# Kernel optimization log

Measured on AMD Instinct MI355X. Metric: run time of the kernel, lower is better.

Reference implementation:

```python
import math
import jax, jax.numpy as jnp
import numpy as np

B, T, C, H = 2, 1024, 1024, 16
D = C // H          # head_dim = 64
ROPE_M = 32         # min(head_dim//2, 64)
FB_M = 32
ROPE_BASE = 10000.0


def setup_inputs() -> dict:
    key = jax.random.key(0)
    ks = jax.random.split(key, 8)
    x = jax.random.normal(ks[0], (B, T, C), dtype=jnp.float32)
    # default coords: per-token position, d_coord=1
    coords = jnp.broadcast_to(jnp.arange(T, dtype=jnp.float32)[None, :, None], (B, T, 1))
    # c_attn / c_proj linear params (torch Linear: y = x @ W.T + b)
    W_attn = jax.random.normal(ks[1], (3 * C, C), dtype=jnp.float32) * (1.0 / math.sqrt(C))
    b_attn = jnp.zeros((3 * C,), dtype=jnp.float32)
    W_proj = jax.random.normal(ks[2], (C, C), dtype=jnp.float32) * (1.0 / math.sqrt(C))
    b_proj = jnp.zeros((C,), dtype=jnp.float32)
    # RoPE freq bank, kind='log': exp(linspace(log(1/base), 0, m)) replicated over d_coord
    steps = jnp.exp(jnp.linspace(math.log(1.0 / ROPE_BASE), 0.0, ROPE_M)).astype(jnp.float32)
    W_rope = steps[:, None]  # [m, d_coord=1]
    # Fourier-bias bank, kind='gaussian', sigma=1.0
    W_fb = jax.random.normal(ks[3], (FB_M, 1), dtype=jnp.float32)
    # betas are zero-init nn.Parameters; use small random values so bias path is exercised
    beta_cos = jax.random.normal(ks[4], (FB_M,), dtype=jnp.float32) * 0.1
    beta_sin = jax.random.normal(ks[5], (FB_M,), dtype=jnp.float32) * 0.1
    return {"x": x, "coords": coords, "W_attn": W_attn, "b_attn": b_attn,
            "W_proj": W_proj, "b_proj": b_proj, "W_rope": W_rope, "W_fb": W_fb,
            "beta_cos": beta_cos, "beta_sin": beta_sin}


def _rope_rotate(z, c, s):
    # z: [B,H,T,D]; c,s: [B,1,T,ROPE_M]; rotates first 2*ROPE_M channels pairwise
    zr = z[..., :2 * ROPE_M].reshape(*z.shape[:-1], ROPE_M, 2)
    y0 = zr[..., 0] * c - zr[..., 1] * s
    y1 = zr[..., 0] * s + zr[..., 1] * c
    y = jnp.stack((y0, y1), axis=-1).reshape(*z.shape[:-1], 2 * ROPE_M)
    return jnp.concatenate([y, z[..., 2 * ROPE_M:]], axis=-1)


def reference(x, coords, W_attn, b_attn, W_proj, b_proj, W_rope, W_fb, beta_cos, beta_sin):
    qkv = x @ W_attn.T + b_attn                      # [B,T,3C]
    q, k, v = jnp.split(qkv, 3, axis=-1)
    to_heads = lambda z: z.reshape(B, T, H, D).transpose(0, 2, 1, 3)  # [B,H,T,D]
    q, k, v = to_heads(q), to_heads(k), to_heads(v)
    # Iron RoPE: theta = coords @ W_rope.T -> [B,T,ROPE_M]
    theta = coords @ W_rope.T
    c = jnp.cos(theta)[:, None]                      # [B,1,T,ROPE_M]
    s = jnp.sin(theta)[:, None]
    q = _rope_rotate(q, c, s)
    k = _rope_rotate(k, c, s)
    att = jnp.einsum('bhqd,bhkd->bhqk', q, k) * (1.0 / math.sqrt(D))
    # relative Fourier bias (shared across heads)
    delta = coords[:, :, None, :] - coords[:, None, :, :]   # [B,Tq,Tk,1]
    S = jnp.einsum('bqkd,md->bqkm', delta, W_fb)            # [B,Tq,Tk,FB_M]
    bias = (jnp.cos(S) * beta_cos + jnp.sin(S) * beta_sin).sum(-1)  # [B,Tq,Tk]
    att = att + (1.0 / math.sqrt(FB_M)) * bias[:, None]     # [B,H,Tq,Tk]
    # non-causal: mask buffer is all ones -> no masking; dropout p=0 -> identity
    att = jax.nn.softmax(att, axis=-1)
    y = jnp.einsum('bhqk,bhkd->bhqd', att, v)
    y = y.transpose(0, 2, 1, 3).reshape(B, T, C)
    y = y @ W_proj.T + b_proj
    return x + y
```

## Files before the change

### kernel.cpp

```cpp
#include <hip/hip_runtime.h>
#include <math.h>

#define Bc 2
#define Tc 1024
#define Cc 1024
#define Hc 16
#define Dc 64
#define DE 128

typedef unsigned short u16;
typedef __attribute__((ext_vector_type(8))) short bf16x8;
typedef __attribute__((ext_vector_type(4))) float f32x4;

#define QSCALE 0.1803368801111243f
#define FIXED_M 24.0f

static __device__ inline u16 f2b(float f) {
    unsigned u = __float_as_uint(f);
    u = (u + 0x7fffu + ((u >> 16) & 1u)) >> 16;
    return (u16)u;
}
static __device__ inline float b2f(u16 h) {
    return __uint_as_float((unsigned)h << 16);
}

typedef __attribute__((address_space(1))) const unsigned int g_u32;
typedef __attribute__((address_space(3))) unsigned int l_u32;
static __device__ __forceinline__ void gll16(const void* g, void* l) {
    __builtin_amdgcn_global_load_lds((g_u32*)g, (l_u32*)l, 16, 0, 0);
}

__global__ __launch_bounds__(256) void cast_all(
    const float* __restrict__ x, const float* __restrict__ wa, const float* __restrict__ wp,
    u16* __restrict__ xb, u16* __restrict__ wab, u16* __restrict__ wpb)
{
    const int NX = Bc * Tc * Cc;
    const int NA = 3 * Cc * Cc;
    int i = (blockIdx.x * 256 + threadIdx.x) * 4;
    const float* src; u16* dst; int off;
    if (i < NX)            { src = x;  dst = xb;  off = i; }
    else if (i < NX + NA)  { src = wa; dst = wab; off = i - NX; }
    else                   { src = wp; dst = wpb; off = i - NX - NA; }
    float4 v = *(const float4*)(src + off);
    ushort4 o;
    o.x = f2b(v.x); o.y = f2b(v.y); o.z = f2b(v.z); o.w = f2b(v.w);
    *(ushort4*)(dst + off) = o;
}

template<int TM, int TN, int WR, int WC, bool OUT_BF16>
__global__ __launch_bounds__(256) void gemm_abt(
    const u16* __restrict__ A, const u16* __restrict__ Bm,
    const float* __restrict__ bias, const float* __restrict__ resid,
    float* __restrict__ outf, u16* __restrict__ outb, int M, int N, int K)
{
    constexpr int WTM = TM / WR;
    constexpr int WTN = TN / WC;
    constexpr int FI = WTM / 16;
    constexpr int FJ = WTN / 16;
    constexpr int ITA = TM / 32;
    constexpr int ITB = TN / 32;
    __shared__ u16 ldsA[2][TM * 64];
    __shared__ u16 ldsB[2][TN * 64];
    const int tid  = threadIdx.x;
    const int wave = tid >> 6;
    const int lane = tid & 63;
    const int l15  = lane & 15;
    const int quad = lane >> 4;
    const int wm = wave / WC;
    const int wn = wave % WC;
    const int tm = blockIdx.y * TM;
    const int tn = blockIdx.x * TN;

    f32x4 acc[FI][FJ] = {};

    auto stage = [&](int buf, int k0) {
#pragma unroll
        for (int it = 0; it < ITA; ++it) {
            int p = it * 256 + tid;
            int row = p >> 3;
            int c = ((p & 7) ^ (row & 7)) * 8;
            gll16(A + (size_t)(tm + row) * K + k0 + c,
                  &ldsA[buf][(it * 256 + (wave << 6)) * 8]);
        }
#pragma unroll
        for (int it = 0; it < ITB; ++it) {
            int p = it * 256 + tid;
            int row = p >> 3;
            int c = ((p & 7) ^ (row & 7)) * 8;
            gll16(Bm + (size_t)(tn + row) * K + k0 + c,
                  &ldsB[buf][(it * 256 + (wave << 6)) * 8]);
        }
    };

    const int NK = K >> 6;
    stage(0, 0);
    for (int ki = 0; ki < NK; ++ki) {
        const int buf = ki & 1;
        __syncthreads();
        if (ki + 1 < NK) stage(buf ^ 1, (ki + 1) << 6);
#pragma unroll
        for (int kk = 0; kk < 2; ++kk) {
            bf16x8 af[FI], bf[FJ];
#pragma unroll
            for (int i = 0; i < FI; ++i) {
                int row = wm * WTM + i * 16 + l15;
                int slot = (kk * 4 + quad) ^ (row & 7);
                af[i] = *(const bf16x8*)&ldsA[buf][row * 64 + slot * 8];
            }
#pragma unroll
            for (int j = 0; j < FJ; ++j) {
                int row = wn * WTN + j * 16 + l15;
                int slot = (kk * 4 + quad) ^ (row & 7);
                bf[j] = *(const bf16x8*)&ldsB[buf][row * 64 + slot * 8];
            }
#pragma unroll
            for (int i = 0; i < FI; ++i)
#pragma unroll
                for (int j = 0; j < FJ; ++j)
                    acc[i][j] = __builtin_amdgcn_mfma_f32_16x16x32_bf16(af[i], bf[j], acc[i][j], 0, 0, 0);
        }
    }

#pragma unroll
    for (int i = 0; i < FI; ++i) {
        int row = tm + wm * WTM + i * 16 + quad * 4;
#pragma unroll
        for (int j = 0; j < FJ; ++j) {
            int col = tn + wn * WTN + j * 16 + l15;
            float bb = bias[col];
#pragma unroll
            for (int r = 0; r < 4; ++r) {
                float v = acc[i][j][r] + bb;
                if (resid) v += resid[(size_t)(row + r) * N + col];
                if (OUT_BF16) outb[(size_t)(row + r) * N + col] = f2b(v);
                else          outf[(size_t)(row + r) * N + col] = v;
            }
        }
    }
}

__global__ __launch_bounds__(256) void prep_kernel(
    const u16* __restrict__ qkv, const float* __restrict__ coords,
    const float* __restrict__ W_rope, const float* __restrict__ W_fb,
    const float* __restrict__ bcos, const float* __restrict__ bsin,
    u16* __restrict__ qe, u16* __restrict__ ke, u16* __restrict__ vt)
{
    const int bt = blockIdx.x;
    const int b = bt >> 10;
    const int t = bt & (Tc - 1);
    const float coord = coords[bt];
    const int tid = threadIdx.x;
    const u16* row = qkv + (size_t)bt * 3072;
    const int e  = tid * 4;
    const int h  = e >> 6;
    const int d0 = e & 63;
    const int m0 = d0 >> 1;

    float th0 = coord * W_rope[m0];
    float th1 = coord * W_rope[m0 + 1];
    float s0 = sinf(th0), c0 = cosf(th0);
    float s1 = sinf(th1), c1 = cosf(th1);

    float q0 = b2f(row[e]), q1 = b2f(row[e + 1]), q2 = b2f(row[e + 2]), q3 = b2f(row[e + 3]);
    float k0 = b2f(row[1024 + e]), k1 = b2f(row[1025 + e]), k2 = b2f(row[1026 + e]), k3 = b2f(row[1027 + e]);
    float v0 = b2f(row[2048 + e]), v1 = b2f(row[2049 + e]), v2 = b2f(row[2050 + e]), v3 = b2f(row[2051 + e]);

    size_t qb = ((size_t)(b * Hc + h) * Tc + t) * DE + d0;
    qe[qb + 0] = f2b((q0 * c0 - q1 * s0) * QSCALE);
    qe[qb + 1] = f2b((q0 * s0 + q1 * c0) * QSCALE);
    qe[qb + 2] = f2b((q2 * c1 - q3 * s1) * QSCALE);
    qe[qb + 3] = f2b((q2 * s1 + q3 * c1) * QSCALE);
    ke[qb + 0] = f2b(k0 * c0 - k1 * s0);
    ke[qb + 1] = f2b(k0 * s0 + k1 * c0);
    ke[qb + 2] = f2b(k2 * c1 - k3 * s1);
    ke[qb + 3] = f2b(k2 * s1 + k3 * c1);

    size_t vb = ((size_t)(b * Hc + h) * Dc + d0) * Tc + t;
    vt[vb]          = f2b(v0);
    vt[vb + Tc]     = f2b(v1);
    vt[vb + 2 * Tc] = f2b(v2);
    vt[vb + 3 * Tc] = f2b(v3);

    {
        const int hh = tid >> 4;
        const int s  = tid & 15;
        const int m  = 2 * s;
        float thf0 = coord * W_fb[m],     thf1 = coord * W_fb[m + 1];
        float sn0 = sinf(thf0), cn0 = cosf(thf0);
        float sn1 = sinf(thf1), cn1 = cosf(thf1);
        float bc0 = bcos[m], bs0 = bsin[m], bc1 = bcos[m + 1], bs1 = bsin[m + 1];
        const float SC = 1.41421356237f * QSCALE;
        unsigned u1 = (unsigned)f2b((bc0 * cn0 + bs0 * sn0) * SC) |
                      ((unsigned)f2b((bc1 * cn1 + bs1 * sn1) * SC) << 16);
        unsigned u2 = (unsigned)f2b((bc0 * sn0 - bs0 * cn0) * SC) |
                      ((unsigned)f2b((bc1 * sn1 - bs1 * cn1) * SC) << 16);
        unsigned cp = (unsigned)f2b(cn0) | ((unsigned)f2b(cn1) << 16);
        unsigned sp = (unsigned)f2b(sn0) | ((unsigned)f2b(sn1) << 16);
        size_t base = ((size_t)(b * Hc + hh) * Tc + t) * DE + 64;
        *(unsigned*)&qe[base + m]      = u1;
        *(unsigned*)&qe[base + 32 + m] = u2;
        *(unsigned*)&ke[base + m]      = cp;
        *(unsigned*)&ke[base + 32 + m] = sp;
    }
}

__global__ __launch_bounds__(256) void attn_kernel(
    const u16* __restrict__ qe, const u16* __restrict__ ke,
    const u16* __restrict__ vt, u16* __restrict__ yb)
{
    __shared__ u16 ldsK[2][64 * 128];
    __shared__ u16 ldsV[2][64 * 64];
    __shared__ u16 plds[4][16][72];
    const int tid  = threadIdx.x;
    const int wave = tid >> 6;
    const int lane = tid & 63;
    const int l15  = lane & 15;
    const int quad = lane >> 4;
    const int qt = blockIdx.x * 64;
    const int h  = blockIdx.y;
    const int b  = blockIdx.z;

    const u16* Q  = qe + ((size_t)(b * Hc + h) * Tc) * DE;
    const u16* Kp = ke + ((size_t)(b * Hc + h) * Tc) * DE;
    const u16* Vp = vt + ((size_t)(b * Hc + h) * Dc) * Tc;

    bf16x8 qf[4];
    {
        const u16* qrow = Q + (size_t)(qt + wave * 16 + l15) * DE + quad * 8;
#pragma unroll
        for (int c = 0; c < 4; ++c) qf[c] = *(const bf16x8*)(qrow + c * 32);
    }

    auto stageKV = [&](int buf, int kt) {
#pragma unroll
        for (int it = 0; it < 4; ++it) {
            int p = it * 256 + tid;
            int row = p >> 4;
            int c = (p & 15) ^ (row & 15);
            gll16(Kp + (size_t)(kt + row) * DE + c * 8,
                  &ldsK[buf][(it * 256 + (wave << 6)) * 8]);
        }
#pragma unroll
        for (int it = 0; it < 2; ++it) {
            int p = it * 256 + tid;
            int row = p >> 3;
            int c = (p & 7) ^ (row & 7);
            gll16(Vp + (size_t)row * Tc + kt + c * 8,
                  &ldsV[buf][(it * 256 + (wave << 6)) * 8]);
        }
    };

    f32x4 o[4] = {};
    float lrow[4] = {0.f, 0.f, 0.f, 0.f};

    stageKV(0, 0);
    for (int ki = 0; ki < Tc / 64; ++ki) {
        const int buf = ki & 1;
        __syncthreads();
        if (ki + 1 < Tc / 64) stageKV(buf ^ 1, (ki + 1) * 64);

        f32x4 sf[4] = {};
#pragma unroll
        for (int f = 0; f < 4; ++f) {
#pragma unroll
            for (int c = 0; c < 4; ++c) {
                int row = f * 16 + l15;
                int slot = (c * 4 + quad) ^ (row & 15);
                bf16x8 kf = *(const bf16x8*)&ldsK[buf][row * 128 + slot * 8];
                sf[f] = __builtin_amdgcn_mfma_f32_16x16x32_bf16(qf[c], kf, sf[f], 0, 0, 0);
            }
        }
        float psum[4] = {0.f, 0.f, 0.f, 0.f};
#pragma unroll
        for (int f = 0; f < 4; ++f)
#pragma unroll
            for (int r = 0; r < 4; ++r) {
                float p = __builtin_amdgcn_exp2f(sf[f][r] - FIXED_M);
                u16 tp = (u16)(__float_as_uint(p) >> 16);
                plds[wave][quad * 4 + r][f * 16 + l15] = tp;
                psum[r] += b2f(tp);
            }
#pragma unroll
        for (int r = 0; r < 4; ++r) {
            float v = psum[r];
#pragma unroll
            for (int off = 1; off < 16; off <<= 1) v += __shfl_xor(v, off);
            lrow[r] += v;
        }

#pragma unroll
        for (int c = 0; c < 2; ++c) {
            bf16x8 pa = *(const bf16x8*)&plds[wave][l15][c * 32 + quad * 8];
#pragma unroll
            for (int df = 0; df < 4; ++df) {
                int row = df * 16 + l15;
                int slot = (c * 4 + quad) ^ (row & 7);
                bf16x8 vf = *(const bf16x8*)&ldsV[buf][row * 64 + slot * 8];
                o[df] = __builtin_amdgcn_mfma_f32_16x16x32_bf16(pa, vf, o[df], 0, 0, 0);
            }
        }
    }

    float rl[4];
#pragma unroll
    for (int r = 0; r < 4; ++r) rl[r] = 1.0f / lrow[r];
#pragma unroll
    for (int df = 0; df < 4; ++df)
#pragma unroll
        for (int r = 0; r < 4; ++r) {
            int t = qt + wave * 16 + quad * 4 + r;
            int d = df * 16 + l15;
            yb[((size_t)b * Tc + t) * Cc + h * Dc + d] = f2b(o[df][r] * rl[r]);
        }
}

extern "C" void kernel_launch(void* const* d_in, const int* in_sizes, int n_in,
                              void* d_out, int out_size, void* d_ws, size_t ws_size,
                              hipStream_t stream) {
    const float* x      = (const float*)d_in[0];
    const float* coords = (const float*)d_in[1];
    const float* W_attn = (const float*)d_in[2];
    const float* b_attn = (const float*)d_in[3];
    const float* W_proj = (const float*)d_in[4];
    const float* b_proj = (const float*)d_in[5];
    const float* W_rope = (const float*)d_in[6];
    const float* W_fb   = (const float*)d_in[7];
    const float* bcos   = (const float*)d_in[8];
    const float* bsin   = (const float*)d_in[9];
    float* out = (float*)d_out;

    char* w = (char*)d_ws;
    const size_t MB = 1024 * 1024;
    u16* xb     = (u16*)(w + 0);
    u16* wab    = (u16*)(w + 4 * MB);
    u16* wpb    = (u16*)(w + 10 * MB);
    u16* qkvb16 = (u16*)(w + 12 * MB);
    u16* qext   = (u16*)(w + 24 * MB);
    u16* kext   = (u16*)(w + 32 * MB);
    u16* vtw    = (u16*)(w + 40 * MB);
    u16* yb     = (u16*)(w + 44 * MB);

    const int NALL = (Bc * Tc * Cc + 3 * Cc * Cc + Cc * Cc) / 4;
    cast_all<<<NALL / 256, 256, 0, stream>>>(x, W_attn, W_proj, xb, wab, wpb);

    dim3 g1(3 * Cc / 128, Bc * Tc / 128);
    gemm_abt<128, 128, 2, 2, true><<<g1, 256, 0, stream>>>(
        xb, wab, b_attn, nullptr, nullptr, qkvb16, Bc * Tc, 3 * Cc, Cc);

    prep_kernel<<<Bc * Tc, 256, 0, stream>>>(qkvb16, coords, W_rope, W_fb, bcos, bsin, qext, kext, vtw);

    dim3 g2(Tc / 64, Hc, Bc);
    attn_kernel<<<g2, 256, 0, stream>>>(qext, kext, vtw, yb);

    dim3 g3(Cc / 64, Bc * Tc / 64);
    gemm_abt<64, 64, 2, 2, false><<<g3, 256, 0, stream>>>(
        yb, wpb, b_proj, x, out, nullptr, Bc * Tc, Cc, Cc);
}
```

Measured before the change: 176.4 us.

## Fuse RoPE and QKV scatter into QKV GEMM epilogue, enlarge proj tile

Moves RoPE rotation, Q scaling and the V transpose into the QKV GEMM epilogue, using a precomputed cos/sin table and a lane shuffle to fetch each pair partner. This removes the intermediate bf16 qkv buffer and the separate prep pass that re-read it. A small prep_tables kernel now builds the rotation table and the Fourier-bias extension columns. The output projection GEMM also moves from 64x64 to 128x64 tiles. The epilogue now issues scattered 2-byte stores into transposed and strided layouts, which may coalesce poorly.

```diff
diff --git a/kernel.cpp b/kernel.cpp
--- a/kernel.cpp
+++ b/kernel.cpp
@@ -47,11 +47,51 @@
     *(ushort4*)(dst + off) = o;
 }
 
-template<int TM, int TN, int WR, int WC, bool OUT_BF16>
+__global__ __launch_bounds__(256) void prep_tables(
+    const float* __restrict__ coords, const float* __restrict__ W_rope,
+    const float* __restrict__ W_fb, const float* __restrict__ bcos,
+    const float* __restrict__ bsin, float2* __restrict__ ctab,
+    u16* __restrict__ qe, u16* __restrict__ ke)
+{
+    const int bt = blockIdx.x;
+    const int b = bt >> 10;
+    const int t = bt & (Tc - 1);
+    const float coord = coords[bt];
+    const int tid = threadIdx.x;
+
+    if (tid < 32) {
+        float th = coord * W_rope[tid];
+        ctab[bt * 32 + tid] = make_float2(cosf(th), sinf(th));
+    }
+
+    const int hh = tid >> 4;
+    const int s  = tid & 15;
+    const int m  = 2 * s;
+    float thf0 = coord * W_fb[m],     thf1 = coord * W_fb[m + 1];
+    float sn0 = sinf(thf0), cn0 = cosf(thf0);
+    float sn1 = sinf(thf1), cn1 = cosf(thf1);
+    float bc0 = bcos[m], bs0 = bsin[m], bc1 = bcos[m + 1], bs1 = bsin[m + 1];
+    const float SC = 1.41421356237f * QSCALE;
+    unsigned u1 = (unsigned)f2b((bc0 * cn0 + bs0 * sn0) * SC) |
+                  ((unsigned)f2b((bc1 * cn1 + bs1 * sn1) * SC) << 16);
+    unsigned u2 = (unsigned)f2b((bc0 * sn0 - bs0 * cn0) * SC) |
+                  ((unsigned)f2b((bc1 * sn1 - bs1 * cn1) * SC) << 16);
+    unsigned cp = (unsigned)f2b(cn0) | ((unsigned)f2b(cn1) << 16);
+    unsigned sp = (unsigned)f2b(sn0) | ((unsigned)f2b(sn1) << 16);
+    size_t base = ((size_t)(b * Hc + hh) * Tc + t) * DE + 64;
+    *(unsigned*)&qe[base + m]      = u1;
+    *(unsigned*)&qe[base + 32 + m] = u2;
+    *(unsigned*)&ke[base + m]      = cp;
+    *(unsigned*)&ke[base + 32 + m] = sp;
+}
+
+template<int TM, int TN, int WR, int WC, int MODE>
 __global__ __launch_bounds__(256) void gemm_abt(
     const u16* __restrict__ A, const u16* __restrict__ Bm,
     const float* __restrict__ bias, const float* __restrict__ resid,
-    float* __restrict__ outf, u16* __restrict__ outb, int M, int N, int K)
+    float* __restrict__ outf, const float2* __restrict__ ctab,
+    u16* __restrict__ qe, u16* __restrict__ ke, u16* __restrict__ vt,
+    int M, int N, int K)
 {
     constexpr int WTM = TM / WR;
     constexpr int WTN = TN / WC;
@@ -121,86 +161,52 @@
         }
     }
 
-#pragma unroll
-    for (int i = 0; i < FI; ++i) {
-        int row = tm + wm * WTM + i * 16 + quad * 4;
-#pragma unroll
-        for (int j = 0; j < FJ; ++j) {
-            int col = tn + wn * WTN + j * 16 + l15;
-            float bb = bias[col];
+    if (MODE == 0) {
+#pragma unroll
+        for (int i = 0; i < FI; ++i) {
+            int row = tm + wm * WTM + i * 16 + quad * 4;
+#pragma unroll
+            for (int j = 0; j < FJ; ++j) {
+                int col = tn + wn * WTN + j * 16 + l15;
+                float bb = bias[col];
+#pragma unroll
+                for (int r = 0; r < 4; ++r) {
+                    float v = acc[i][j][r] + bb;
+                    if (resid) v += resid[(size_t)(row + r) * N + col];
+                    outf[(size_t)(row + r) * N + col] = v;
+                }
+            }
+        }
+    } else {
+        const int sec = tn >> 10;
+#pragma unroll
+        for (int i = 0; i < FI; ++i) {
 #pragma unroll
             for (int r = 0; r < 4; ++r) {
-                float v = acc[i][j][r] + bb;
-                if (resid) v += resid[(size_t)(row + r) * N + col];
-                if (OUT_BF16) outb[(size_t)(row + r) * N + col] = f2b(v);
-                else          outf[(size_t)(row + r) * N + col] = v;
-            }
-        }
-    }
-}
-
-__global__ __launch_bounds__(256) void prep_kernel(
-    const u16* __restrict__ qkv, const float* __restrict__ coords,
-    const float* __restrict__ W_rope, const float* __restrict__ W_fb,
-    const float* __restrict__ bcos, const float* __restrict__ bsin,
-    u16* __restrict__ qe, u16* __restrict__ ke, u16* __restrict__ vt)
-{
-    const int bt = blockIdx.x;
-    const int b = bt >> 10;
-    const int t = bt & (Tc - 1);
-    const float coord = coords[bt];
-    const int tid = threadIdx.x;
-    const u16* row = qkv + (size_t)bt * 3072;
-    const int e  = tid * 4;
-    const int h  = e >> 6;
-    const int d0 = e & 63;
-    const int m0 = d0 >> 1;
-
-    float th0 = coord * W_rope[m0];
-    float th1 = coord * W_rope[m0 + 1];
-    float s0 = sinf(th0), c0 = cosf(th0);
-    float s1 = sinf(th1), c1 = cosf(th1);
-
-    float q0 = b2f(row[e]), q1 = b2f(row[e + 1]), q2 = b2f(row[e + 2]), q3 = b2f(row[e + 3]);
-    float k0 = b2f(row[1024 + e]), k1 = b2f(row[1025 + e]), k2 = b2f(row[1026 + e]), k3 = b2f(row[1027 + e]);
-    float v0 = b2f(row[2048 + e]), v1 = b2f(row[2049 + e]), v2 = b2f(row[2050 + e]), v3 = b2f(row[2051 + e]);
-
-    size_t qb = ((size_t)(b * Hc + h) * Tc + t) * DE + d0;
-    qe[qb + 0] = f2b((q0 * c0 - q1 * s0) * QSCALE);
-    qe[qb + 1] = f2b((q0 * s0 + q1 * c0) * QSCALE);
-    qe[qb + 2] = f2b((q2 * c1 - q3 * s1) * QSCALE);
-    qe[qb + 3] = f2b((q2 * s1 + q3 * c1) * QSCALE);
-    ke[qb + 0] = f2b(k0 * c0 - k1 * s0);
-    ke[qb + 1] = f2b(k0 * s0 + k1 * c0);
-    ke[qb + 2] = f2b(k2 * c1 - k3 * s1);
-    ke[qb + 3] = f2b(k2 * s1 + k3 * c1);
-
-    size_t vb = ((size_t)(b * Hc + h) * Dc + d0) * Tc + t;
-    vt[vb]          = f2b(v0);
-    vt[vb + Tc]     = f2b(v1);
-    vt[vb + 2 * Tc] = f2b(v2);
-    vt[vb + 3 * Tc] = f2b(v3);
-
-    {
-        const int hh = tid >> 4;
-        const int s  = tid & 15;
-        const int m  = 2 * s;
-        float thf0 = coord * W_fb[m],     thf1 = coord * W_fb[m + 1];
-        float sn0 = sinf(thf0), cn0 = cosf(thf0);
-        float sn1 = sinf(thf1), cn1 = cosf(thf1);
-        float bc0 = bcos[m], bs0 = bsin[m], bc1 = bcos[m + 1], bs1 = bsin[m + 1];
-        const float SC = 1.41421356237f * QSCALE;
-        unsigned u1 = (unsigned)f2b((bc0 * cn0 + bs0 * sn0) * SC) |
-                      ((unsigned)f2b((bc1 * cn1 + bs1 * sn1) * SC) << 16);
-        unsigned u2 = (unsigned)f2b((bc0 * sn0 - bs0 * cn0) * SC) |
-                      ((unsigned)f2b((bc1 * sn1 - bs1 * cn1) * SC) << 16);
-        unsigned cp = (unsigned)f2b(cn0) | ((unsigned)f2b(cn1) << 16);
-        unsigned sp = (unsigned)f2b(sn0) | ((unsigned)f2b(sn1) << 16);
-        size_t base = ((size_t)(b * Hc + hh) * Tc + t) * DE + 64;
-        *(unsigned*)&qe[base + m]      = u1;
-        *(unsigned*)&qe[base + 32 + m] = u2;
-        *(unsigned*)&ke[base + m]      = cp;
-        *(unsigned*)&ke[base + 32 + m] = sp;
+                int grow = tm + wm * WTM + i * 16 + quad * 4 + r;
+                int b = grow >> 10, tl = grow & (Tc - 1);
+#pragma unroll
+                for (int j = 0; j < FJ; ++j) {
+                    int col = tn + wn * WTN + j * 16 + l15;
+                    int cw = col & (Cc - 1);
+                    int h = cw >> 6, d = cw & 63;
+                    float v = acc[i][j][r] + bias[col];
+                    if (sec == 2) {
+                        vt[((size_t)(b * Hc + h) * Dc + d) * Tc + tl] = f2b(v);
+                    } else {
+                        float2 cs = ctab[grow * 32 + (d >> 1)];
+                        float p = __shfl_xor(v, 1);
+                        float rot = (d & 1) ? (p * cs.y + v * cs.x)
+                                            : (v * cs.x - p * cs.y);
+                        if (sec == 0) {
+                            qe[((size_t)(b * Hc + h) * Tc + tl) * DE + d] = f2b(rot * QSCALE);
+                        } else {
+                            ke[((size_t)(b * Hc + h) * Tc + tl) * DE + d] = f2b(rot);
+                        }
+                    }
+                }
+            }
+        }
     }
 }
 
@@ -331,28 +337,31 @@
 
     char* w = (char*)d_ws;
     const size_t MB = 1024 * 1024;
-    u16* xb     = (u16*)(w + 0);
-    u16* wab    = (u16*)(w + 4 * MB);
-    u16* wpb    = (u16*)(w + 10 * MB);
-    u16* qkvb16 = (u16*)(w + 12 * MB);
-    u16* qext   = (u16*)(w + 24 * MB);
-    u16* kext   = (u16*)(w + 32 * MB);
-    u16* vtw    = (u16*)(w + 40 * MB);
-    u16* yb     = (u16*)(w + 44 * MB);
+    u16*    xb   = (u16*)(w + 0);
+    u16*    wab  = (u16*)(w + 4 * MB);
+    u16*    wpb  = (u16*)(w + 10 * MB);
+    float2* ctab = (float2*)(w + 12 * MB);
+    u16*    qext = (u16*)(w + 13 * MB);
+    u16*    kext = (u16*)(w + 21 * MB);
+    u16*    vtw  = (u16*)(w + 29 * MB);
+    u16*    yb   = (u16*)(w + 33 * MB);
 
     const int NALL = (Bc * Tc * Cc + 3 * Cc * Cc + Cc * Cc) / 4;
     cast_all<<<NALL / 256, 256, 0, stream>>>(x, W_attn, W_proj, xb, wab, wpb);
 
+    prep_tables<<<Bc * Tc, 256, 0, stream>>>(coords, W_rope, W_fb, bcos, bsin,
+                                             ctab, qext, kext);
+
     dim3 g1(3 * Cc / 128, Bc * Tc / 128);
-    gemm_abt<128, 128, 2, 2, true><<<g1, 256, 0, stream>>>(
-        xb, wab, b_attn, nullptr, nullptr, qkvb16, Bc * Tc, 3 * Cc, Cc);
-
-    prep_kernel<<<Bc * Tc, 256, 0, stream>>>(qkvb16, coords, W_rope, W_fb, bcos, bsin, qext, kext, vtw);
+    gemm_abt<128, 128, 2, 2, 1><<<g1, 256, 0, stream>>>(
+        xb, wab, b_attn, nullptr, nullptr, ctab, qext, kext, vtw,
+        Bc * Tc, 3 * Cc, Cc);
 
     dim3 g2(Tc / 64, Hc, Bc);
     attn_kernel<<<g2, 256, 0, stream>>>(qext, kext, vtw, yb);
 
-    dim3 g3(Cc / 64, Bc * Tc / 64);
-    gemm_abt<64, 64, 2, 2, false><<<g3, 256, 0, stream>>>(
-        yb, wpb, b_proj, x, out, nullptr, Bc * Tc, Cc, Cc);
-}
+    dim3 g3(Cc / 64, Bc * Tc / 128);
+    gemm_abt<128, 64, 2, 2, 0><<<g3, 256, 0, stream>>>(
+        yb, wpb, b_proj, x, out, nullptr, nullptr, nullptr, nullptr,
+        Bc * Tc, Cc, Cc);
+}
```

Measured after the change: 185.7 us. 1.05x slower.
